# Performance work log

Hardware: AMD Instinct MI355X
Metric: run time of the kernel (lower is better)

Reference implementation:

```python
import jax, jax.numpy as jnp
import numpy as np
import math

DK = 768  # latent_size used for the scale (not the per-head dim, matching the original)

def setup_inputs() -> dict:
    key = jax.random.key(0)
    k1, k2, k3 = jax.random.split(key, 3)
    B, H, S, D = 4, 12, 2048, 64
    queries = jax.random.normal(k1, (B, H, S, D), dtype=jnp.float32)
    keys = jax.random.normal(k2, (B, H, S, D), dtype=jnp.float32)
    values = jax.random.normal(k3, (B, S, H, D), dtype=jnp.float32)  # note [B,S,H,D] layout
    return {"queries": queries, "keys": keys, "values": values}

def reference(queries, keys, values):
    # scores: [B,H,S,S]
    scores = jnp.einsum('bhqd,bhkd->bhqk', queries, keys) / math.sqrt(DK)
    probs = jax.nn.softmax(scores, axis=3)
    v = jnp.transpose(values, (0, 2, 1, 3))  # [B,S,H,D] -> [B,H,S,D]
    return jnp.einsum('bhqk,bhkd->bhqd', probs, v)
```

## Files before the change

kernel.cpp:

```cpp
#include <hip/hip_runtime.h>

#define SQ 2048
#define DH 64
#define NH 12
#define NBH 48
#define QTILE 128
#define KTILE 64
#define NITER (SQ / KTILE)
#define NQT (SQ / QTILE)

#define KB0 0
#define KB1 8192
#define VB0 16384
#define VB1 24576

typedef short short8 __attribute__((ext_vector_type(8)));
typedef float f32x2  __attribute__((ext_vector_type(2)));
typedef float f32x4  __attribute__((ext_vector_type(4)));
typedef float f32x16 __attribute__((ext_vector_type(16)));
typedef int   i32x2 __attribute__((ext_vector_type(2)));
typedef int   i32x4 __attribute__((ext_vector_type(4)));

#define MFMA32(a, b, c) __builtin_amdgcn_mfma_f32_32x32x16_bf16(a, b, c, 0, 0, 0)

typedef __attribute__((address_space(1))) const void* gas_ptr;
typedef __attribute__((address_space(3))) void* las_ptr;

__device__ __forceinline__ void load_lds16(const void* g, void* l) {
    __builtin_amdgcn_global_load_lds((gas_ptr)g, (las_ptr)l, 16, 0, 0);
}

#if defined(__has_builtin) && __has_builtin(__builtin_amdgcn_cvt_pk_bf16_f32)
typedef __bf16 bf16x2_t __attribute__((ext_vector_type(2)));
__device__ __forceinline__ unsigned pk2bf(float a, float b) {
    bf16x2_t v = __builtin_amdgcn_cvt_pk_bf16_f32(a, b);
    union { bf16x2_t v; unsigned u; } c; c.v = v; return c.u;
}
#else
__device__ __forceinline__ unsigned pk2bf(float a, float b) {
    union { float f; unsigned u; } x, y; x.f = a; y.f = b;
    unsigned ra = x.u + 0x7FFFu + ((x.u >> 16) & 1u);
    unsigned rb = y.u + 0x7FFFu + ((y.u >> 16) & 1u);
    return (ra >> 16) | (rb & 0xFFFF0000u);
}
#endif

#ifdef __has_builtin
#if __has_builtin(__builtin_amdgcn_permlane32_swap)
#define HAVE_PLSWAP 1
#else
#define HAVE_PLSWAP 0
#endif
#else
#define HAVE_PLSWAP 0
#endif

#define KCONV_BLOCKS (NBH * SQ * DH / 8 / 256)
__global__ __launch_bounds__(256)
void prepass(const float* __restrict__ K, short* __restrict__ Kb,
             const float* __restrict__ V, short* __restrict__ Vt) {
    __shared__ float Ls[64][68];
    if (blockIdx.x < KCONV_BLOCKS) {
        const size_t i = (size_t)(blockIdx.x * 256 + threadIdx.x) * 8;
        f32x4 a = *(const f32x4*)&K[i];
        f32x4 b = *(const f32x4*)&K[i + 4];
        unsigned o[4] = { pk2bf(a[0], a[1]), pk2bf(a[2], a[3]),
                          pk2bf(b[0], b[1]), pk2bf(b[2], b[3]) };
        *(i32x4*)&Kb[i] = *(i32x4*)o;
        return;
    }
    const int bx = blockIdx.x - KCONV_BLOCKS;
    const int st = bx & 31;
    const int bh = bx >> 5;
    const int b = bh / NH, h = bh % NH;
    const int s0 = st * 64;
    const float* src = V + ((size_t)b * SQ * NH + (size_t)h) * DH;
    const int dg = threadIdx.x & 15;
    const int sl = threadIdx.x >> 4;
    #pragma unroll
    for (int p = 0; p < 4; ++p) {
        const int row = p * 16 + sl;
        *(f32x4*)&Ls[row][dg * 4] =
            *(const f32x4*)&src[(size_t)(s0 + row) * (NH * DH) + dg * 4];
    }
    __syncthreads();
    const int dr = threadIdx.x >> 2;
    const int sc = (threadIdx.x & 3) * 16;
    unsigned out[8];
    #pragma unroll
    for (int jj = 0; jj < 8; ++jj)
        out[jj] = pk2bf(Ls[sc + 2 * jj][dr], Ls[sc + 2 * jj + 1][dr]);
    short* dst = Vt + (size_t)bh * DH * SQ + (size_t)dr * SQ + s0 + sc;
    *(i32x4*)(dst)     = *(i32x4*)&out[0];
    *(i32x4*)(dst + 8) = *(i32x4*)&out[4];
}

__global__ __launch_bounds__(256, 3)
void attn_fused_kernel(const float* __restrict__ Q,
                       const short* __restrict__ Kb,
                       const short* __restrict__ Vtg,
                       float* __restrict__ O) {
    __shared__ __align__(16) char L[32768];

    const int tid  = threadIdx.x;
    const int lane = tid & 63;
    const int w    = tid >> 6;
    const int m31  = lane & 31;
    const int hl   = lane >> 5;
    const int l7   = lane & 7;

    const int bx  = blockIdx.x;
    const int xcd = bx & 7;
    const int i96 = bx >> 3;
    const int bh  = xcd * 6 + (i96 % 6);
    const int qt  = i96 / 6;
    const int q0 = qt * QTILE;

    const float* Qb  = Q   + (size_t)bh * SQ * DH;
    const short* Kbh = Kb  + (size_t)bh * SQ * DH;
    const short* Vbh = Vtg + (size_t)bh * DH * SQ;
    float*       Ob  = O   + (size_t)bh * SQ * DH;

    const float qscale = 0.03608439182435161f * 1.4426950408889634f;

    short8 qf[4];
    {
        const int qrow = q0 + 32 * w + m31;
        #pragma unroll
        for (int s = 0; s < 4; ++s) {
            const float* src = Qb + (size_t)qrow * DH + 16 * s + 8 * hl;
            f32x4 qa = *(const f32x4*)src;
            f32x4 qb = *(const f32x4*)(src + 4);
            union { unsigned u[4]; short8 v; } f;
            f.u[0] = pk2bf(qa[0] * qscale, qa[1] * qscale);
            f.u[1] = pk2bf(qa[2] * qscale, qa[3] * qscale);
            f.u[2] = pk2bf(qb[0] * qscale, qb[1] * qscale);
            f.u[3] = pk2bf(qb[2] * qscale, qb[3] * qscale);
            qf[s] = f.v;
        }
    }

    const int gk = (lane & 7) ^ (lane >> 3);
    const int rr = w * 8 + (lane >> 3);
    const short* kg0 = Kbh + (size_t)rr * DH + gk * 8;
    const short* kg1 = kg0 + 32 * DH;
    const short* vg0 = Vbh + (size_t)rr * SQ + gk * 8;
    const short* vg1 = vg0 + 32 * SQ;
    const int wslot = w * 1024;

    int aoff[4];
    #pragma unroll
    for (int s = 0; s < 4; ++s) aoff[s] = m31 * 128 + (((2 * s + hl) ^ l7) * 16);

    f32x16 o0 = {}, o1 = {};
    f32x16 sn0, sn1;
    short8 pfc[4];
    f32x2 lp2 = {0.f, 0.f};

    auto issueK = [&](int kb, int t) {
        const short* p0 = kg0 + (size_t)t * (KTILE * DH);
        const short* p1 = kg1 + (size_t)t * (KTILE * DH);
        load_lds16(p0, L + kb + wslot);
        load_lds16(p1, L + kb + 4096 + wslot);
    };
    auto issueV = [&](int vb, int t) {
        const short* p0 = vg0 + (size_t)t * KTILE;
        const short* p1 = vg1 + (size_t)t * KTILE;
        load_lds16(p0, L + vb + wslot);
        load_lds16(p1, L + vb + 4096 + wslot);
    };

    auto qk = [&](int kb) {
        f32x16 a0 = {}, a1 = {};
        #pragma unroll
        for (int s = 0; s < 4; ++s) {
            short8 ka0 = *(const short8*)(L + kb + aoff[s]);
            short8 ka1 = *(const short8*)(L + kb + 4096 + aoff[s]);
            a0 = MFMA32(ka0, qf[s], a0);
            a1 = MFMA32(ka1, qf[s], a1);
        }
        sn0 = a0; sn1 = a1;
    };

    auto softmax_pack = [&](const f32x16& sv, short8* dst) {
        #pragma unroll
        for (int wd = 0; wd < 2; ++wd) {
            float p[8];
            #pragma unroll
            for (int j = 0; j < 8; ++j)
                p[j] = __builtin_amdgcn_exp2f(sv[8 * wd + j]);
            f32x2 s01 = {p[0], p[1]}, s23 = {p[2], p[3]};
            f32x2 s45 = {p[4], p[5]}, s67 = {p[6], p[7]};
            lp2 += (s01 + s23) + (s45 + s67);
            unsigned a0 = pk2bf(p[0], p[1]);
            unsigned a1 = pk2bf(p[2], p[3]);
            unsigned b0 = pk2bf(p[4], p[5]);
            unsigned b1 = pk2bf(p[6], p[7]);
            union { unsigned u[4]; short8 v; } fr;
#if HAVE_PLSWAP
            i32x2 r0 = __builtin_amdgcn_permlane32_swap((int)a0, (int)b0, false, false);
            i32x2 r1 = __builtin_amdgcn_permlane32_swap((int)a1, (int)b1, false, false);
            fr.u[0] = (unsigned)r0.x;
            fr.u[1] = (unsigned)r1.x;
            fr.u[2] = (unsigned)r0.y;
            fr.u[3] = (unsigned)r1.y;
#else
            unsigned r0 = (unsigned)__shfl_xor((int)(hl ? a0 : b0), 32, 64);
            unsigned r1 = (unsigned)__shfl_xor((int)(hl ? a1 : b1), 32, 64);
            fr.u[0] = hl ? r0 : a0;
            fr.u[1] = hl ? r1 : a1;
            fr.u[2] = hl ? b0 : r0;
            fr.u[3] = hl ? b1 : r1;
#endif
            dst[wd] = fr.v;
        }
    };
    auto softmax2 = [&]() {
        softmax_pack(sn0, &pfc[0]);
        softmax_pack(sn1, &pfc[2]);
    };

    auto pv = [&](int vb) {
        #pragma unroll
        for (int s = 0; s < 4; ++s) {
            short8 vv0 = *(const short8*)(L + vb + aoff[s]);
            short8 vv1 = *(const short8*)(L + vb + 4096 + aoff[s]);
            o0 = MFMA32(pfc[s], vv0, o0);
            o1 = MFMA32(pfc[s], vv1, o1);
        }
    };

    issueK(KB0, 0); issueV(VB0, 0); issueK(KB1, 1);
    __syncthreads();
    qk(KB0);
    softmax2();

    #pragma unroll 1
    for (int t = 0; t < NITER - 2; t += 2) {
        __syncthreads();
        issueK(KB0, t + 2);
        issueV(VB1, t + 1);
        qk(KB1);
        pv(VB0);
        softmax2();
        __syncthreads();
        issueK(KB1, t + 3);
        issueV(VB0, t + 2);
        qk(KB0);
        pv(VB1);
        softmax2();
    }

    __syncthreads();
    issueV(VB1, NITER - 1);
    qk(KB1);
    pv(VB0);
    softmax2();
    __syncthreads();
    pv(VB1);

    float lp = lp2.x + lp2.y;
    float v = lp;
    v += __shfl_xor(v, 32, 64);
    const float linv = 1.0f / v;

    #pragma unroll
    for (int dt = 0; dt < 2; ++dt) {
        const f32x16& o = dt ? o1 : o0;
        #pragma unroll
        for (int reg = 0; reg < 16; ++reg) {
            const int qp = (reg & 3) + 8 * (reg >> 2) + 4 * hl;
            const float rl = __shfl(linv, qp, 64);
            const int q = q0 + 32 * w + qp;
            Ob[(size_t)q * DH + 32 * dt + m31] = o[reg] * rl;
        }
    }
}

extern "C" void kernel_launch(void* const* d_in, const int* in_sizes, int n_in,
                              void* d_out, int out_size, void* d_ws, size_t ws_size,
                              hipStream_t stream) {
    const float* Q = (const float*)d_in[0];
    const float* K = (const float*)d_in[1];
    const float* V = (const float*)d_in[2];
    float* O = (float*)d_out;

    short* Kb  = (short*)d_ws;
    short* Vtg = Kb + (size_t)NBH * SQ * DH;

    prepass<<<dim3(KCONV_BLOCKS + NBH * 32), dim3(256), 0, stream>>>(K, Kb, V, Vtg);
    attn_fused_kernel<<<dim3(NBH * NQT), dim3(256), 0, stream>>>(Q, Kb, Vtg, O);
}
```

Measured before the change: 174.1 us.

## Raise occupancy target and reorder tile step with MFMA priority boost

Raises the launch-bounds occupancy hint from 3 to 4 waves per SIMD, which forces the compiler to fit the kernel into fewer registers. It reorders each tile step to issue PV before QK and splits QK into two sequential accumulators so fewer live registers are needed. The MFMA section is wrapped in s_setprio so this wave's matrix work is favoured over other waves. The row-sum accumulator is split into two chains to shorten the dependency chain. The tighter register budget risks spills, and the new ordering changes how MFMA and exp work overlap across waves.

```diff
diff --git a/kernel.cpp b/kernel.cpp
--- a/kernel.cpp
+++ b/kernel.cpp
@@ -95,7 +95,7 @@
     *(i32x4*)(dst + 8) = *(i32x4*)&out[4];
 }
 
-__global__ __launch_bounds__(256, 3)
+__global__ __launch_bounds__(256, 4)
 void attn_fused_kernel(const float* __restrict__ Q,
                        const short* __restrict__ Kb,
                        const short* __restrict__ Vtg,
@@ -155,7 +155,8 @@
     f32x16 o0 = {}, o1 = {};
     f32x16 sn0, sn1;
     short8 pfc[4];
-    f32x2 lp2 = {0.f, 0.f};
+    f32x2 lpa = {0.f, 0.f};
+    f32x2 lpb = {0.f, 0.f};
 
     auto issueK = [&](int kb, int t) {
         const short* p0 = kg0 + (size_t)t * (KTILE * DH);
@@ -170,16 +171,19 @@
         load_lds16(p1, L + vb + 4096 + wslot);
     };
 
-    auto qk = [&](int kb) {
-        f32x16 a0 = {}, a1 = {};
-        #pragma unroll
-        for (int s = 0; s < 4; ++s) {
-            short8 ka0 = *(const short8*)(L + kb + aoff[s]);
-            short8 ka1 = *(const short8*)(L + kb + 4096 + aoff[s]);
-            a0 = MFMA32(ka0, qf[s], a0);
-            a1 = MFMA32(ka1, qf[s], a1);
-        }
-        sn0 = a0; sn1 = a1;
+    auto qk_h0 = [&](int kb) {
+        f32x16 a = {};
+        #pragma unroll
+        for (int s = 0; s < 4; ++s)
+            a = MFMA32(*(const short8*)(L + kb + aoff[s]), qf[s], a);
+        sn0 = a;
+    };
+    auto qk_h1 = [&](int kb) {
+        f32x16 a = {};
+        #pragma unroll
+        for (int s = 0; s < 4; ++s)
+            a = MFMA32(*(const short8*)(L + kb + 4096 + aoff[s]), qf[s], a);
+        sn1 = a;
     };
 
     auto softmax_pack = [&](const f32x16& sv, short8* dst) {
@@ -191,7 +195,8 @@
                 p[j] = __builtin_amdgcn_exp2f(sv[8 * wd + j]);
             f32x2 s01 = {p[0], p[1]}, s23 = {p[2], p[3]};
             f32x2 s45 = {p[4], p[5]}, s67 = {p[6], p[7]};
-            lp2 += (s01 + s23) + (s45 + s67);
+            lpa += (s01 + s23);
+            lpb += (s45 + s67);
             unsigned a0 = pk2bf(p[0], p[1]);
             unsigned a1 = pk2bf(p[2], p[3]);
             unsigned b0 = pk2bf(p[4], p[5]);
@@ -215,10 +220,6 @@
             dst[wd] = fr.v;
         }
     };
-    auto softmax2 = [&]() {
-        softmax_pack(sn0, &pfc[0]);
-        softmax_pack(sn1, &pfc[2]);
-    };
 
     auto pv = [&](int vb) {
         #pragma unroll
@@ -230,36 +231,41 @@
         }
     };
 
+    auto tile_step = [&](int kb_rd, int vb_rd) {
+        __builtin_amdgcn_s_setprio(1);
+        pv(vb_rd);
+        qk_h0(kb_rd);
+        qk_h1(kb_rd);
+        __builtin_amdgcn_s_setprio(0);
+        softmax_pack(sn0, &pfc[0]);
+        softmax_pack(sn1, &pfc[2]);
+    };
+
     issueK(KB0, 0); issueV(VB0, 0); issueK(KB1, 1);
     __syncthreads();
-    qk(KB0);
-    softmax2();
+    qk_h0(KB0); qk_h1(KB0);
+    softmax_pack(sn0, &pfc[0]);
+    softmax_pack(sn1, &pfc[2]);
 
     #pragma unroll 1
     for (int t = 0; t < NITER - 2; t += 2) {
         __syncthreads();
         issueK(KB0, t + 2);
         issueV(VB1, t + 1);
-        qk(KB1);
-        pv(VB0);
-        softmax2();
+        tile_step(KB1, VB0);
         __syncthreads();
         issueK(KB1, t + 3);
         issueV(VB0, t + 2);
-        qk(KB0);
-        pv(VB1);
-        softmax2();
+        tile_step(KB0, VB1);
     }
 
     __syncthreads();
     issueV(VB1, NITER - 1);
-    qk(KB1);
-    pv(VB0);
-    softmax2();
+    tile_step(KB1, VB0);
     __syncthreads();
     pv(VB1);
 
-    float lp = lp2.x + lp2.y;
+    float lp = (lpa.x + lpa.y) + (lpb.x + lpb.y);
     float v = lp;
     v += __shfl_xor(v, 32, 64);
     const float linv = 1.0f / v;
```

Result: no change. 173.1 us (-0.6%).

## Split KV tile across wave pairs with two query groups per wave

Applied to the files above, without the earlier changes.

Each wave now handles 64 query rows as two 32-row groups and only half of each 64-key tile. A K fragment read from LDS is reused for two query groups, and V fragments are reused across both groups, which cuts LDS read traffic per MFMA. Partial softmax denominators and output accumulators from the two waves of a pair are combined through LDS at the end. This costs twice the accumulator registers, extra barriers and an LDS reduction step, and may lower occupancy under the 3-blocks launch bound.

```diff
diff --git a/kernel.cpp b/kernel.cpp
--- a/kernel.cpp
+++ b/kernel.cpp
@@ -105,6 +105,8 @@
     const int tid  = threadIdx.x;
     const int lane = tid & 63;
     const int w    = tid >> 6;
+    const int wq   = w >> 1;
+    const int wk   = w & 1;
     const int m31  = lane & 31;
     const int hl   = lane >> 5;
     const int l7   = lane & 7;
@@ -123,9 +125,10 @@
 
     const float qscale = 0.03608439182435161f * 1.4426950408889634f;
 
-    short8 qf[4];
-    {
-        const int qrow = q0 + 32 * w + m31;
+    short8 qfA[4], qfB[4];
+    #pragma unroll
+    for (int g = 0; g < 2; ++g) {
+        const int qrow = q0 + wq * 64 + g * 32 + m31;
         #pragma unroll
         for (int s = 0; s < 4; ++s) {
             const float* src = Qb + (size_t)qrow * DH + 16 * s + 8 * hl;
@@ -136,7 +139,7 @@
             f.u[1] = pk2bf(qa[2] * qscale, qa[3] * qscale);
             f.u[2] = pk2bf(qb[0] * qscale, qb[1] * qscale);
             f.u[3] = pk2bf(qb[2] * qscale, qb[3] * qscale);
-            qf[s] = f.v;
+            if (g == 0) qfA[s] = f.v; else qfB[s] = f.v;
         }
     }
 
@@ -148,14 +151,21 @@
     const short* vg1 = vg0 + 32 * SQ;
     const int wslot = w * 1024;
 
-    int aoff[4];
-    #pragma unroll
-    for (int s = 0; s < 4; ++s) aoff[s] = m31 * 128 + (((2 * s + hl) ^ l7) * 16);
-
-    f32x16 o0 = {}, o1 = {};
-    f32x16 sn0, sn1;
-    short8 pfc[4];
-    f32x2 lp2 = {0.f, 0.f};
+    int koff[4];
+    #pragma unroll
+    for (int s = 0; s < 4; ++s)
+        koff[s] = wk * 4096 + m31 * 128 + (((2 * s + hl) ^ l7) * 16);
+    int voff[2];
+    #pragma unroll
+    for (int sp = 0; sp < 2; ++sp)
+        voff[sp] = m31 * 128 + (((4 * wk + 2 * sp + hl) ^ l7) * 16);
+
+    f32x16 oc[4];
+    #pragma unroll
+    for (int i = 0; i < 4; ++i) oc[i] = (f32x16){};
+    f32x16 snA, snB;
+    short8 pfA[2], pfB[2];
+    f32x2 lp[2] = {{0.f, 0.f}, {0.f, 0.f}};
 
     auto issueK = [&](int kb, int t) {
         const short* p0 = kg0 + (size_t)t * (KTILE * DH);
@@ -171,18 +181,17 @@
     };
 
     auto qk = [&](int kb) {
-        f32x16 a0 = {}, a1 = {};
+        f32x16 a = {}, b = {};
         #pragma unroll
         for (int s = 0; s < 4; ++s) {
-            short8 ka0 = *(const short8*)(L + kb + aoff[s]);
-            short8 ka1 = *(const short8*)(L + kb + 4096 + aoff[s]);
-            a0 = MFMA32(ka0, qf[s], a0);
-            a1 = MFMA32(ka1, qf[s], a1);
-        }
-        sn0 = a0; sn1 = a1;
-    };
-
-    auto softmax_pack = [&](const f32x16& sv, short8* dst) {
+            short8 ka = *(const short8*)(L + kb + koff[s]);
+            a = MFMA32(ka, qfA[s], a);
+            b = MFMA32(ka, qfB[s], b);
+        }
+        snA = a; snB = b;
+    };
+
+    auto softmax_pack = [&](const f32x16& sv, short8* dst, int gi) {
         #pragma unroll
         for (int wd = 0; wd < 2; ++wd) {
             float p[8];
@@ -191,7 +200,7 @@
                 p[j] = __builtin_amdgcn_exp2f(sv[8 * wd + j]);
             f32x2 s01 = {p[0], p[1]}, s23 = {p[2], p[3]};
             f32x2 s45 = {p[4], p[5]}, s67 = {p[6], p[7]};
-            lp2 += (s01 + s23) + (s45 + s67);
+            lp[gi] += (s01 + s23) + (s45 + s67);
             unsigned a0 = pk2bf(p[0], p[1]);
             unsigned a1 = pk2bf(p[2], p[3]);
             unsigned b0 = pk2bf(p[4], p[5]);
@@ -215,25 +224,24 @@
             dst[wd] = fr.v;
         }
     };
-    auto softmax2 = [&]() {
-        softmax_pack(sn0, &pfc[0]);
-        softmax_pack(sn1, &pfc[2]);
-    };
 
     auto pv = [&](int vb) {
         #pragma unroll
-        for (int s = 0; s < 4; ++s) {
-            short8 vv0 = *(const short8*)(L + vb + aoff[s]);
-            short8 vv1 = *(const short8*)(L + vb + 4096 + aoff[s]);
-            o0 = MFMA32(pfc[s], vv0, o0);
-            o1 = MFMA32(pfc[s], vv1, o1);
+        for (int sp = 0; sp < 2; ++sp) {
+            short8 v0 = *(const short8*)(L + vb + voff[sp]);
+            short8 v1 = *(const short8*)(L + vb + 4096 + voff[sp]);
+            oc[0] = MFMA32(pfA[sp], v0, oc[0]);
+            oc[1] = MFMA32(pfA[sp], v1, oc[1]);
+            oc[2] = MFMA32(pfB[sp], v0, oc[2]);
+            oc[3] = MFMA32(pfB[sp], v1, oc[3]);
         }
     };
 
     issueK(KB0, 0); issueV(VB0, 0); issueK(KB1, 1);
     __syncthreads();
     qk(KB0);
-    softmax2();
+    softmax_pack(snA, pfA, 0);
+    softmax_pack(snB, pfB, 1);
 
     #pragma unroll 1
     for (int t = 0; t < NITER - 2; t += 2) {
@@ -242,37 +250,68 @@
         issueV(VB1, t + 1);
         qk(KB1);
         pv(VB0);
-        softmax2();
+        softmax_pack(snA, pfA, 0);
+        softmax_pack(snB, pfB, 1);
         __syncthreads();
         issueK(KB1, t + 3);
         issueV(VB0, t + 2);
         qk(KB0);
         pv(VB1);
-        softmax2();
+        softmax_pack(snA, pfA, 0);
+        softmax_pack(snB, pfB, 1);
     }
 
     __syncthreads();
     issueV(VB1, NITER - 1);
     qk(KB1);
     pv(VB0);
-    softmax2();
+    softmax_pack(snA, pfA, 0);
+    softmax_pack(snB, pfB, 1);
     __syncthreads();
     pv(VB1);
 
-    float lp = lp2.x + lp2.y;
-    float v = lp;
-    v += __shfl_xor(v, 32, 64);
-    const float linv = 1.0f / v;
-
-    #pragma unroll
-    for (int dt = 0; dt < 2; ++dt) {
-        const f32x16& o = dt ? o1 : o0;
-        #pragma unroll
-        for (int reg = 0; reg < 16; ++reg) {
-            const int qp = (reg & 3) + 8 * (reg >> 2) + 4 * hl;
-            const float rl = __shfl(linv, qp, 64);
-            const int q = q0 + 32 * w + qp;
-            Ob[(size_t)q * DH + 32 * dt + m31] = o[reg] * rl;
+    float lA = lp[0].x + lp[0].y;  lA += __shfl_xor(lA, 32, 64);
+    float lB = lp[1].x + lp[1].y;  lB += __shfl_xor(lB, 32, 64);
+
+    __syncthreads();
+    if (lane < 32) {
+        *(float*)(L + ((w * 2 + 0) * 32 + m31) * 4) = lA;
+        *(float*)(L + ((w * 2 + 1) * 32 + m31) * 4) = lB;
+    }
+    __syncthreads();
+    {
+        const int pw = w ^ 1;
+        lA += *(const float*)(L + ((pw * 2 + 0) * 32 + m31) * 4);
+        lB += *(const float*)(L + ((pw * 2 + 1) * 32 + m31) * 4);
+    }
+    const float linvA = 1.0f / lA;
+    const float linvB = 1.0f / lB;
+
+    __syncthreads();
+    if (wk == 1) {
+        #pragma unroll
+        for (int i = 0; i < 4; ++i)
+            *(f32x16*)(L + wq * 16384 + i * 4096 + lane * 64) = oc[i];
+    }
+    __syncthreads();
+    if (wk == 0) {
+        f32x16 pr[4];
+        #pragma unroll
+        for (int i = 0; i < 4; ++i)
+            pr[i] = *(const f32x16*)(L + wq * 16384 + i * 4096 + lane * 64);
+        #pragma unroll
+        for (int grp = 0; grp < 2; ++grp) {
+            #pragma unroll
+            for (int dt = 0; dt < 2; ++dt) {
+                #pragma unroll
+                for (int reg = 0; reg < 16; ++reg) {
+                    const int qp = (reg & 3) + 8 * (reg >> 2) + 4 * hl;
+                    const float rl = __shfl(grp ? linvB : linvA, qp, 64);
+                    const int q = q0 + wq * 64 + grp * 32 + qp;
+                    const float val = oc[grp * 2 + dt][reg] + pr[grp * 2 + dt][reg];
+                    Ob[(size_t)q * DH + 32 * dt + m31] = val * rl;
+                }
+            }
         }
     }
 }
```

Measured after the change: 196.5 us. +12.8%, slower.
